# Optimization experiments

Hardware: AMD Instinct MI355X
Metric: run time of the kernel (lower is better)

## Reference

```python
import jax, jax.numpy as jnp
import numpy as np

B, S, D = 32, 2048, 512


def setup_inputs() -> dict:
    key = jax.random.key(0)
    k1, k2, k3, k4 = jax.random.split(key, 4)
    hidden = jax.random.normal(k1, (B, 1, D), dtype=jnp.float32)
    enc_outputs = jax.random.normal(k2, (B, S, D), dtype=jnp.float32)
    # nn.Linear(dim_context, dim_context) params, scaled like torch default init
    W = jax.random.normal(k3, (D, D), dtype=jnp.float32) * (1.0 / np.sqrt(D))
    b = jax.random.normal(k4, (D,), dtype=jnp.float32) * (1.0 / np.sqrt(D))
    return {"hidden": hidden, "enc_outputs": enc_outputs, "W": W, "b": b}


def reference(hidden, enc_outputs, W, b):
    # Batched equivalent of the per-timestep loop:
    #   energy_i = Linear(enc_outputs[:, i, :])            -> [B, D]
    #   score_i  = bmm(hidden [B,1,D], energy_i.T [B,D,1]) -> [B, 1]
    # Fused: one linear over all timesteps + one contraction.
    energy = jnp.einsum("bsd,ed->bse", enc_outputs, W) + b      # [B, S, D]
    attn_energies = jnp.einsum("bd,bsd->bs", hidden[:, 0, :], energy)  # [B, S]
    return jax.nn.softmax(attn_energies, axis=-1)[:, None, :]   # [B, 1, S]
```

## Files before the change

### kernel.cpp

```cpp
#include <hip/hip_runtime.h>
#include <math.h>

#define BB 32
#define SS 2048
#define DD 512
#define ECHUNKS 8
#define SBLOCKS 64

__global__ void __launch_bounds__(256) compute_u_partial(
    const float* __restrict__ hidden, const float* __restrict__ W,
    float* __restrict__ part) {
    const int k = blockIdx.x;
    const int b = blockIdx.y;
    __shared__ float h_s[DD / ECHUNKS];
    if (threadIdx.x < DD / ECHUNKS)
        h_s[threadIdx.x] = hidden[b * DD + k * (DD / ECHUNKS) + threadIdx.x];
    __syncthreads();

    const int t = threadIdx.x;
    float acc0 = 0.f, acc1 = 0.f;
    const float2* W2 = (const float2*)W;
    #pragma unroll 8
    for (int i = 0; i < DD / ECHUNKS; ++i) {
        const int e = k * (DD / ECHUNKS) + i;
        const float he = h_s[i];
        const float2 w = W2[(size_t)e * (DD / 2) + t];
        acc0 = fmaf(he, w.x, acc0);
        acc1 = fmaf(he, w.y, acc1);
    }
    ((float2*)(part + (size_t)(k * BB + b) * DD))[t] = make_float2(acc0, acc1);
}

__global__ void __launch_bounds__(256) scores_kernel(
    const float* __restrict__ enc, const float* __restrict__ part,
    float* __restrict__ logits) {
    const int b    = blockIdx.y;
    const int lane = threadIdx.x & 63;
    const int wv   = threadIdx.x >> 6;

    float4 u0 = make_float4(0.f, 0.f, 0.f, 0.f);
    float4 u1 = make_float4(0.f, 0.f, 0.f, 0.f);
    #pragma unroll
    for (int k = 0; k < ECHUNKS; ++k) {
        const float4* pk = (const float4*)(part + (size_t)(k * BB + b) * DD);
        const float4 a = pk[lane * 2 + 0];
        const float4 c = pk[lane * 2 + 1];
        u0.x += a.x; u0.y += a.y; u0.z += a.z; u0.w += a.w;
        u1.x += c.x; u1.y += c.y; u1.z += c.z; u1.w += c.w;
    }

    const int waves_per_b = SBLOCKS * 4;
    const int wave_id     = blockIdx.x * 4 + wv;
    const float4* encb = (const float4*)(enc + (size_t)b * SS * DD);

    #pragma unroll 2
    for (int k = 0; k < SS / (SBLOCKS * 4); k += 2) {
        const int s0 = wave_id + k * waves_per_b;
        const int s1 = s0 + waves_per_b;
        const float4* r0 = encb + (size_t)s0 * (DD / 4);
        const float4* r1 = encb + (size_t)s1 * (DD / 4);
        float4 a0 = r0[lane * 2 + 0];
        float4 a1 = r0[lane * 2 + 1];
        float4 c0 = r1[lane * 2 + 0];
        float4 c1 = r1[lane * 2 + 1];
        float acc0 = a0.x * u0.x + a0.y * u0.y + a0.z * u0.z + a0.w * u0.w
                   + a1.x * u1.x + a1.y * u1.y + a1.z * u1.z + a1.w * u1.w;
        float acc1 = c0.x * u0.x + c0.y * u0.y + c0.z * u0.z + c0.w * u0.w
                   + c1.x * u1.x + c1.y * u1.y + c1.z * u1.z + c1.w * u1.w;
        #pragma unroll
        for (int off = 32; off > 0; off >>= 1) {
            acc0 += __shfl_xor(acc0, off, 64);
            acc1 += __shfl_xor(acc1, off, 64);
        }
        if (lane == 0) {
            logits[b * SS + s0] = acc0;
            logits[b * SS + s1] = acc1;
        }
    }
}

__global__ void __launch_bounds__(512) softmax_kernel(float* __restrict__ io) {
    const int b = blockIdx.x;
    const int t = threadIdx.x;
    const int lane = t & 63, wv = t >> 6;
    float4* p = (float4*)(io + b * SS);

    float4 v = p[t];
    float m = fmaxf(fmaxf(v.x, v.y), fmaxf(v.z, v.w));
    #pragma unroll
    for (int off = 32; off > 0; off >>= 1)
        m = fmaxf(m, __shfl_xor(m, off, 64));

    __shared__ float red_m[8];
    __shared__ float red_s[8];
    if (lane == 0) red_m[wv] = m;
    __syncthreads();
    m = red_m[0];
    #pragma unroll
    for (int i = 1; i < 8; ++i) m = fmaxf(m, red_m[i]);

    v.x = __expf(v.x - m);
    v.y = __expf(v.y - m);
    v.z = __expf(v.z - m);
    v.w = __expf(v.w - m);
    float sum = v.x + v.y + v.z + v.w;
    #pragma unroll
    for (int off = 32; off > 0; off >>= 1)
        sum += __shfl_xor(sum, off, 64);
    if (lane == 0) red_s[wv] = sum;
    __syncthreads();
    sum = 0.f;
    #pragma unroll
    for (int i = 0; i < 8; ++i) sum += red_s[i];

    const float inv = 1.f / sum;
    v.x *= inv; v.y *= inv; v.z *= inv; v.w *= inv;
    p[t] = v;
}

extern "C" void kernel_launch(void* const* d_in, const int* in_sizes, int n_in,
                              void* d_out, int out_size, void* d_ws, size_t ws_size,
                              hipStream_t stream) {
    const float* hidden = (const float*)d_in[0];
    const float* enc    = (const float*)d_in[1];
    const float* W      = (const float*)d_in[2];
    float* out  = (float*)d_out;
    float* part = (float*)d_ws;

    compute_u_partial<<<dim3(ECHUNKS, BB), dim3(256), 0, stream>>>(hidden, W, part);
    scores_kernel<<<dim3(SBLOCKS, BB), dim3(256), 0, stream>>>(enc, part, out);
    softmax_kernel<<<dim3(BB), dim3(512), 0, stream>>>(out);
}
```

Baseline: 34.56 us.

## Fuse online-softmax partial max/sum into scores kernel, split normalize across blocks

The scores kernel now computes per-block running max and exp-sum of its logits (online softmax partials) and writes them to workspace. The final softmax kernel is replaced by a normalize kernel that combines the 64 partials per batch with a wave reduction and rescales logits, using two blocks per batch instead of one. This removes the block-wide max/sum reductions from the tail kernel and spreads it over more blocks, at the cost of extra exp work and a syncthreads in the scores kernel.

```diff
diff --git a/kernel.cpp b/kernel.cpp
--- a/kernel.cpp
+++ b/kernel.cpp
@@ -33,7 +33,7 @@
 
 __global__ void __launch_bounds__(256) scores_kernel(
     const float* __restrict__ enc, const float* __restrict__ part,
-    float* __restrict__ logits) {
+    float* __restrict__ logits, float2* __restrict__ partials) {
     const int b    = blockIdx.y;
     const int lane = threadIdx.x & 63;
     const int wv   = threadIdx.x >> 6;
@@ -53,9 +53,10 @@
     const int wave_id     = blockIdx.x * 4 + wv;
     const float4* encb = (const float4*)(enc + (size_t)b * SS * DD);
 
-    #pragma unroll 2
-    for (int k = 0; k < SS / (SBLOCKS * 4); k += 2) {
-        const int s0 = wave_id + k * waves_per_b;
+    float rv[8];
+    #pragma unroll
+    for (int kk = 0; kk < 4; ++kk) {
+        const int s0 = wave_id + (2 * kk) * waves_per_b;
         const int s1 = s0 + waves_per_b;
         const float4* r0 = encb + (size_t)s0 * (DD / 4);
         const float4* r1 = encb + (size_t)s1 * (DD / 4);
@@ -72,50 +73,57 @@
             acc0 += __shfl_xor(acc0, off, 64);
             acc1 += __shfl_xor(acc1, off, 64);
         }
+        rv[2 * kk]     = acc0;
+        rv[2 * kk + 1] = acc1;
         if (lane == 0) {
             logits[b * SS + s0] = acc0;
             logits[b * SS + s1] = acc1;
         }
     }
+
+    float mw = rv[0];
+    #pragma unroll
+    for (int i = 1; i < 8; ++i) mw = fmaxf(mw, rv[i]);
+    float sw = 0.f;
+    #pragma unroll
+    for (int i = 0; i < 8; ++i) sw += __expf(rv[i] - mw);
+
+    __shared__ float2 wred[4];
+    if (lane == 0) wred[wv] = make_float2(mw, sw);
+    __syncthreads();
+    if (threadIdx.x == 0) {
+        float2 p0 = wred[0], p1 = wred[1], p2 = wred[2], p3 = wred[3];
+        float mb = fmaxf(fmaxf(p0.x, p1.x), fmaxf(p2.x, p3.x));
+        float sb = p0.y * __expf(p0.x - mb) + p1.y * __expf(p1.x - mb)
+                 + p2.y * __expf(p2.x - mb) + p3.y * __expf(p3.x - mb);
+        partials[b * SBLOCKS + blockIdx.x] = make_float2(mb, sb);
+    }
 }
 
-__global__ void __launch_bounds__(512) softmax_kernel(float* __restrict__ io) {
-    const int b = blockIdx.x;
-    const int t = threadIdx.x;
-    const int lane = t & 63, wv = t >> 6;
-    float4* p = (float4*)(io + b * SS);
+__global__ void __launch_bounds__(256) normalize_kernel(
+    float* __restrict__ logits, const float2* __restrict__ partials) {
+    const int b    = blockIdx.y;
+    const int lane = threadIdx.x & 63;
 
-    float4 v = p[t];
-    float m = fmaxf(fmaxf(v.x, v.y), fmaxf(v.z, v.w));
+    const float2 pl = partials[b * SBLOCKS + lane];
+    float m = pl.x;
     #pragma unroll
     for (int off = 32; off > 0; off >>= 1)
         m = fmaxf(m, __shfl_xor(m, off, 64));
-
-    __shared__ float red_m[8];
-    __shared__ float red_s[8];
-    if (lane == 0) red_m[wv] = m;
-    __syncthreads();
-    m = red_m[0];
-    #pragma unroll
-    for (int i = 1; i < 8; ++i) m = fmaxf(m, red_m[i]);
-
-    v.x = __expf(v.x - m);
-    v.y = __expf(v.y - m);
-    v.z = __expf(v.z - m);
-    v.w = __expf(v.w - m);
-    float sum = v.x + v.y + v.z + v.w;
+    float s = pl.y * __expf(pl.x - m);
     #pragma unroll
     for (int off = 32; off > 0; off >>= 1)
-        sum += __shfl_xor(sum, off, 64);
-    if (lane == 0) red_s[wv] = sum;
-    __syncthreads();
-    sum = 0.f;
-    #pragma unroll
-    for (int i = 0; i < 8; ++i) sum += red_s[i];
+        s += __shfl_xor(s, off, 64);
+    const float inv = 1.f / s;
 
-    const float inv = 1.f / sum;
-    v.x *= inv; v.y *= inv; v.z *= inv; v.w *= inv;
-    p[t] = v;
+    float4* p = (float4*)(logits + b * SS);
+    const int idx = blockIdx.x * 256 + threadIdx.x;
+    float4 v = p[idx];
+    v.x = __expf(v.x - m) * inv;
+    v.y = __expf(v.y - m) * inv;
+    v.z = __expf(v.z - m) * inv;
+    v.w = __expf(v.w - m) * inv;
+    p[idx] = v;
 }
 
 extern "C" void kernel_launch(void* const* d_in, const int* in_sizes, int n_in,
@@ -126,8 +134,9 @@
     const float* W      = (const float*)d_in[2];
     float* out  = (float*)d_out;
     float* part = (float*)d_ws;
+    float2* partials = (float2*)((char*)d_ws + (size_t)ECHUNKS * BB * DD * sizeof(float));
 
     compute_u_partial<<<dim3(ECHUNKS, BB), dim3(256), 0, stream>>>(hidden, W, part);
-    scores_kernel<<<dim3(SBLOCKS, BB), dim3(256), 0, stream>>>(enc, part, out);
-    softmax_kernel<<<dim3(BB), dim3(512), 0, stream>>>(out);
+    scores_kernel<<<dim3(SBLOCKS, BB), dim3(256), 0, stream>>>(enc, part, out, partials);
+    normalize_kernel<<<dim3(2, BB), dim3(256), 0, stream>>>(out, partials);
 }
```

New measurement: 33.83 us. 2.1% less time.
